# Kernel tuning notes

Hardware: AMD Instinct MI355X
Metric: run time of the kernel (lower is better)

The kernel has to match this reference:

```python
import jax, jax.numpy as jnp
import numpy as np

B = 12288
C = 1000


def setup_inputs() -> dict:
    key = jax.random.key(0)
    k1, k2 = jax.random.split(key)
    pred = jax.random.normal(k1, (B, C), dtype=jnp.float32)
    target = jax.random.randint(k2, (B,), 0, C)
    return {"pred": pred, "target": target, "num_classes": C}


def reference(pred, target, num_classes):
    # Vectorized form of the per-class loop: for a pair (b=negative, a=positive),
    # only class i = target[a] contributes, provided target[b] != target[a].
    #   margin[b, a] = pred[a, target[a]] - pred[b, target[a]]
    #   weight[b, a] = 1 / (N[target[b]] * N[target[a]])
    # loss = sum(hinge(margin) * weight) / (E * (E - 1)), E = #classes with N>0.
    N = jnp.zeros((num_classes,), jnp.float32).at[target].add(1.0)  # per-class counts
    E = jnp.sum(N > 0).astype(jnp.float32)  # exist_class_num
    f_own = jnp.take_along_axis(pred, target[:, None], axis=1)[:, 0]  # [B] pred[a, t[a]]
    P = pred[:, target]                      # [B, B]; P[b, a] = pred[b, target[a]]
    margin = f_own[None, :] - P              # [B_neg, B_pos]
    Nt = N[target]                            # [B] N[t[.]] (>= 1 always)
    diff = target[:, None] != target[None, :]  # t[b] != t[a]
    w = jnp.where(diff, 1.0 / (Nt[:, None] * Nt[None, :]), 0.0)
    loss = jnp.sum(jnp.maximum(1.0 - margin, 0.0) * w) / (E * (E - 1.0))
    return loss.reshape(1)
```

## Files before the change

kernel.cpp:

```cpp
#include <hip/hip_runtime.h>
#include <float.h>


#define CCLS 1000
#define PAD 64
#define LSLOT 32
#define TPB 1024
#define CCH 250
#define NCH 4
#define NRBLK 128
#define LSTR 257

__global__ __launch_bounds__(1024) void k_prep(const int* __restrict__ target, int B,
        int* ncnt, float* invN, int* fill, float* scal, int* flags) {
    __shared__ int h[CCLS];
    __shared__ int esh, mx;
    int tid = threadIdx.x;
    if (tid < CCLS) h[tid] = 0;
    if (tid == 0) { esh = 0; mx = 0; }
    __syncthreads();
    for (int j = tid; j < B; j += TPB) atomicAdd(&h[target[j]], 1);
    __syncthreads();
    if (tid < CCLS) {
        int n = h[tid];
        ncnt[tid] = n;
        invN[tid] = n ? 1.0f / (float)n : 0.f;
        fill[tid] = 0;
        if (n) atomicAdd(&esh, 1);
        atomicMax(&mx, n);
    }
    __syncthreads();
    if (tid == 0) {
        scal[0] = (float)esh;
        scal[1] = 0.f;
        flags[0] = 0;
        flags[1] = (mx > LSLOT - 1) ? 1 : 0;
    }
}

__global__ void k_scatter(const float* __restrict__ pred, const int* __restrict__ target,
                          int* fill, float* thrP, int B) {
    int j = blockIdx.x * 256 + threadIdx.x;
    if (j >= B) return;
    int tj = target[j];
    float fo = pred[(size_t)j * CCLS + tj];
    int pos = atomicAdd(&fill[tj], 1);
    if (pos < PAD) thrP[tj * PAD + pos] = fo - 1.0f;
}

__global__ __launch_bounds__(256) void k_sortpfx(const int* __restrict__ ncnt,
                                                 float* thrP, float* prefP) {
    int c = (blockIdx.x * 256 + threadIdx.x) >> 6;
    int lane = threadIdx.x & 63;
    if (c >= CCLS) return;
    int cnt = min(ncnt[c], PAD - 1);
    int base = c * PAD;
    float v = (lane < cnt) ? thrP[base + lane] : FLT_MAX;
    int rank = 0;
    float psum = 0.f, tot = 0.f;
    for (int k = 0; k < cnt; ++k) {
        float u = __shfl(v, k);
        bool sm = (u < v) || (u == v && k < lane);
        rank += sm ? 1 : 0;
        psum += sm ? u : 0.f;
        tot += u;
    }
    if (lane < cnt) { thrP[base + rank] = v; prefP[base + rank] = psum; }
    else           { thrP[base + lane] = FLT_MAX; prefP[base + lane] = tot; }
}

__global__ __launch_bounds__(TPB) void k_main(const float* __restrict__ pred,
        const int* __restrict__ target,
        const float* __restrict__ thrP, const float* __restrict__ prefP,
        const float* __restrict__ invN,
        float* scal, int* flags, float* __restrict__ out, int B, int RPB) {
    __shared__ float thrL[LSLOT][LSTR];
    __shared__ float prefL[LSLOT][LSTR];
    __shared__ float invNL[CCLS];
    __shared__ float redL[TPB / 64];

    const int tid = threadIdx.x;
    const int chunk = blockIdx.x / NRBLK;
    const int rblk = blockIdx.x % NRBLK;
    const int c0 = chunk * CCH;
    const int rbase = rblk * RPB;
    const int ovf = flags[1];

    for (int k = tid; k < CCLS; k += TPB) invNL[k] = invN[k];
    for (int g = tid; g < CCH * LSLOT; g += TPB) {
        int cc = g >> 5, k = g & 31;
        thrL[k][cc] = thrP[(size_t)(c0 + cc) * PAD + k];
        prefL[k][cc] = prefP[(size_t)(c0 + cc) * PAD + k];
    }
    __syncthreads();

    const int rr = tid >> 8;
    const int cc = tid & 255;
    const bool cvalid = cc < CCH;
    const int ccS = cvalid ? cc : 0;
    const int c = c0 + ccS;
    const float invc = cvalid ? invNL[c] : 0.f;

    const int rows = min(RPB, B - rbase);
    const int nit = (rows > rr) ? ((rows - rr + 3) >> 2) : 0;

    float acc = 0.f;
    if (!ovf) {
        const float e15 = thrL[15][ccS];
        const float e7  = thrL[7][ccS],  e23 = thrL[23][ccS];
        const float e3  = thrL[3][ccS],  e11 = thrL[11][ccS];
        const float e19 = thrL[19][ccS], e27 = thrL[27][ccS];
        const float e1  = thrL[1][ccS],  e5  = thrL[5][ccS];
        const float e9  = thrL[9][ccS],  e13 = thrL[13][ccS];
        const float e17 = thrL[17][ccS], e21 = thrL[21][ccS];
        const float e25 = thrL[25][ccS], e29 = thrL[29][ccS];
#pragma unroll 4
        for (int it = 0; it < nit; ++it) {
            const int i = rbase + it * 4 + rr;
            const int ti = target[i];
            const float p = pred[(size_t)i * CCLS + c];
            const bool b1 = e15 < p;
            const float t2 = b1 ? e23 : e7;
            const bool b2 = t2 < p;
            const float t3 = b1 ? (b2 ? e27 : e19) : (b2 ? e11 : e3);
            const bool b3 = t3 < p;
            const float t4 = b1 ? (b2 ? (b3 ? e29 : e25) : (b3 ? e21 : e17))
                                : (b2 ? (b3 ? e13 : e9)  : (b3 ? e5  : e1));
            const bool b4 = t4 < p;
            int lo = (b1 ? 16 : 0) + (b2 ? 8 : 0) + (b3 ? 4 : 0) + (b4 ? 2 : 0);
            lo += (thrL[lo][ccS] < p) ? 1 : 0;
            const float contrib = (float)lo * p - prefL[lo][ccS];
            const float w = (c != ti) ? invc * invNL[ti] : 0.f;
            acc = fmaf(contrib, w, acc);
        }
    } else {
        const float* seg = thrP + (size_t)c * PAD;
        const float* pseg = prefP + (size_t)c * PAD;
        for (int it = 0; it < nit; ++it) {
            const int i = rbase + it * 4 + rr;
            const int ti = target[i];
            const float p = pred[(size_t)i * CCLS + c];
            int lo = 0;
#pragma unroll
            for (int s = 32; s; s >>= 1) lo += (seg[lo + s - 1] < p) ? s : 0;
            const float contrib = (float)lo * p - pseg[lo];
            const float w = (c != ti) ? invc * invNL[ti] : 0.f;
            acc = fmaf(contrib, w, acc);
        }
    }

    for (int o = 32; o; o >>= 1) acc += __shfl_down(acc, o);
    if ((tid & 63) == 0) redL[tid >> 6] = acc;
    __syncthreads();
    if (tid == 0) {
        float ssum = 0.f;
#pragma unroll
        for (int k = 0; k < TPB / 64; ++k) ssum += redL[k];
        atomicAdd(&scal[1], ssum);
        __threadfence();
        int done = atomicAdd(&flags[0], 1);
        if (done == (int)gridDim.x - 1) {
            float tot = atomicAdd(&scal[1], 0.f);
            float E = scal[0];
            out[0] = tot / (E * (E - 1.0f));
        }
    }
}

extern "C" void kernel_launch(void* const* d_in, const int* in_sizes, int n_in,
                              void* d_out, int out_size, void* d_ws, size_t ws_size,
                              hipStream_t stream) {
    const float* pred = (const float*)d_in[0];
    const int* target = (const int*)d_in[1];
    const int B = in_sizes[1];

    char* ws = (char*)d_ws;
    int* ncnt    = (int*)(ws + 0);
    float* invN  = (float*)(ws + 4096);
    int* fill    = (int*)(ws + 8192);
    float* scal  = (float*)(ws + 12288);
    int* flags   = (int*)(ws + 12352);
    float* thrP  = (float*)(ws + 16384);
    float* prefP = (float*)(ws + 16384 + 262144);

    const int gb = (B + 255) / 256;
    const int RPB = (B + NRBLK - 1) / NRBLK;

    k_prep<<<1, TPB, 0, stream>>>(target, B, ncnt, invN, fill, scal, flags);
    k_scatter<<<gb, 256, 0, stream>>>(pred, target, fill, thrP, B);
    k_sortpfx<<<(CCLS * 64 + 255) / 256, 256, 0, stream>>>(ncnt, thrP, prefP);
    k_main<<<NCH * NRBLK, TPB, 0, stream>>>(pred, target, thrP, prefP, invN,
                                            scal, flags, (float*)d_out, B, RPB);
}
```

Measured before the change: 49.30 us.

## Interleave thresholds and prefix sums as float2, stage per-row weights in LDS

Thresholds and prefix sums are stored together as float2 pairs, so the final search step and the prefix lookup come from adjacent LDS slots. Per-row target and inverse count are staged once per block in shared memory instead of being reloaded from global memory each iteration. The main loop is manually batched four rows at a time, issuing all pred loads before the tree searches for more memory-level parallelism. Risks are higher register pressure and larger LDS use, and rows per block are capped at RMAX=256.

```diff
diff --git a/kernel.cpp b/kernel.cpp
--- a/kernel.cpp
+++ b/kernel.cpp
@@ -10,6 +10,7 @@
 #define NCH 4
 #define NRBLK 128
 #define LSTR 257
+#define RMAX 256
 
 __global__ __launch_bounds__(1024) void k_prep(const int* __restrict__ target, int B,
         int* ncnt, float* invN, int* fill, float* scal, int* flags) {
@@ -39,23 +40,23 @@
 }
 
 __global__ void k_scatter(const float* __restrict__ pred, const int* __restrict__ target,
-                          int* fill, float* thrP, int B) {
+                          int* fill, float2* pairP, int B) {
     int j = blockIdx.x * 256 + threadIdx.x;
     if (j >= B) return;
     int tj = target[j];
     float fo = pred[(size_t)j * CCLS + tj];
     int pos = atomicAdd(&fill[tj], 1);
-    if (pos < PAD) thrP[tj * PAD + pos] = fo - 1.0f;
+    if (pos < PAD) pairP[tj * PAD + pos] = make_float2(fo - 1.0f, 0.f);
 }
 
 __global__ __launch_bounds__(256) void k_sortpfx(const int* __restrict__ ncnt,
-                                                 float* thrP, float* prefP) {
+                                                 float2* pairP) {
     int c = (blockIdx.x * 256 + threadIdx.x) >> 6;
     int lane = threadIdx.x & 63;
     if (c >= CCLS) return;
     int cnt = min(ncnt[c], PAD - 1);
     int base = c * PAD;
-    float v = (lane < cnt) ? thrP[base + lane] : FLT_MAX;
+    float v = (lane < cnt) ? pairP[base + lane].x : FLT_MAX;
     int rank = 0;
     float psum = 0.f, tot = 0.f;
     for (int k = 0; k < cnt; ++k) {
@@ -65,18 +66,16 @@
         psum += sm ? u : 0.f;
         tot += u;
     }
-    if (lane < cnt) { thrP[base + rank] = v; prefP[base + rank] = psum; }
-    else           { thrP[base + lane] = FLT_MAX; prefP[base + lane] = tot; }
+    if (lane < cnt) pairP[base + rank] = make_float2(v, psum);
+    else            pairP[base + lane] = make_float2(FLT_MAX, tot);
 }
 
 __global__ __launch_bounds__(TPB) void k_main(const float* __restrict__ pred,
-        const int* __restrict__ target,
-        const float* __restrict__ thrP, const float* __restrict__ prefP,
+        const int* __restrict__ target, const float2* __restrict__ pairP,
         const float* __restrict__ invN,
         float* scal, int* flags, float* __restrict__ out, int B, int RPB) {
-    __shared__ float thrL[LSLOT][LSTR];
-    __shared__ float prefL[LSLOT][LSTR];
-    __shared__ float invNL[CCLS];
+    __shared__ float2 pairL[LSLOT][LSTR];
+    __shared__ float2 rowWT[RMAX];
     __shared__ float redL[TPB / 64];
 
     const int tid = threadIdx.x;
@@ -85,12 +84,15 @@
     const int c0 = chunk * CCH;
     const int rbase = rblk * RPB;
     const int ovf = flags[1];
-
-    for (int k = tid; k < CCLS; k += TPB) invNL[k] = invN[k];
+    const int rows = min(min(RPB, B - rbase), RMAX);
+
     for (int g = tid; g < CCH * LSLOT; g += TPB) {
         int cc = g >> 5, k = g & 31;
-        thrL[k][cc] = thrP[(size_t)(c0 + cc) * PAD + k];
-        prefL[k][cc] = prefP[(size_t)(c0 + cc) * PAD + k];
+        pairL[k][cc] = pairP[(size_t)(c0 + cc) * PAD + k];
+    }
+    for (int r = tid; r < rows; r += TPB) {
+        int t = target[rbase + r];
+        rowWT[r] = make_float2(__int_as_float(t), invN[t]);
     }
     __syncthreads();
 
@@ -99,26 +101,23 @@
     const bool cvalid = cc < CCH;
     const int ccS = cvalid ? cc : 0;
     const int c = c0 + ccS;
-    const float invc = cvalid ? invNL[c] : 0.f;
-
-    const int rows = min(RPB, B - rbase);
-    const int nit = (rows > rr) ? ((rows - rr + 3) >> 2) : 0;
+    const float invc = cvalid ? invN[c] : 0.f;
 
     float acc = 0.f;
     if (!ovf) {
-        const float e15 = thrL[15][ccS];
-        const float e7  = thrL[7][ccS],  e23 = thrL[23][ccS];
-        const float e3  = thrL[3][ccS],  e11 = thrL[11][ccS];
-        const float e19 = thrL[19][ccS], e27 = thrL[27][ccS];
-        const float e1  = thrL[1][ccS],  e5  = thrL[5][ccS];
-        const float e9  = thrL[9][ccS],  e13 = thrL[13][ccS];
-        const float e17 = thrL[17][ccS], e21 = thrL[21][ccS];
-        const float e25 = thrL[25][ccS], e29 = thrL[29][ccS];
-#pragma unroll 4
-        for (int it = 0; it < nit; ++it) {
-            const int i = rbase + it * 4 + rr;
-            const int ti = target[i];
-            const float p = pred[(size_t)i * CCLS + c];
+        float e1  = pairL[1][ccS].x,  e3  = pairL[3][ccS].x;
+        float e5  = pairL[5][ccS].x,  e7  = pairL[7][ccS].x;
+        float e9  = pairL[9][ccS].x,  e11 = pairL[11][ccS].x;
+        float e13 = pairL[13][ccS].x, e15 = pairL[15][ccS].x;
+        float e17 = pairL[17][ccS].x, e19 = pairL[19][ccS].x;
+        float e21 = pairL[21][ccS].x, e23 = pairL[23][ccS].x;
+        float e25 = pairL[25][ccS].x, e27 = pairL[27][ccS].x;
+        float e29 = pairL[29][ccS].x;
+        asm volatile("" : "+v"(e1), "+v"(e3), "+v"(e5), "+v"(e7), "+v"(e9),
+                          "+v"(e11), "+v"(e13), "+v"(e15), "+v"(e17), "+v"(e19),
+                          "+v"(e21), "+v"(e23), "+v"(e25), "+v"(e27), "+v"(e29));
+
+        auto tree = [&](float p) -> int {
             const bool b1 = e15 < p;
             const float t2 = b1 ? e23 : e7;
             const bool b2 = t2 < p;
@@ -127,24 +126,55 @@
             const float t4 = b1 ? (b2 ? (b3 ? e29 : e25) : (b3 ? e21 : e17))
                                 : (b2 ? (b3 ? e13 : e9)  : (b3 ? e5  : e1));
             const bool b4 = t4 < p;
-            int lo = (b1 ? 16 : 0) + (b2 ? 8 : 0) + (b3 ? 4 : 0) + (b4 ? 2 : 0);
-            lo += (thrL[lo][ccS] < p) ? 1 : 0;
-            const float contrib = (float)lo * p - prefL[lo][ccS];
-            const float w = (c != ti) ? invc * invNL[ti] : 0.f;
-            acc = fmaf(contrib, w, acc);
+            return (b1 ? 16 : 0) + (b2 ? 8 : 0) + (b3 ? 4 : 0) + (b4 ? 2 : 0);
+        };
+        auto fin = [&](float p, int lo, float2 qa, float2 qb, float2 wt) -> float {
+            const bool b5 = qa.x < p;
+            const float lof = (float)lo + (b5 ? 1.f : 0.f);
+            const float pf = b5 ? qb.y : qa.y;
+            const float contrib = lof * p - pf;
+            const int ti = __float_as_int(wt.x);
+            const float w = (c != ti) ? invc * wt.y : 0.f;
+            return contrib * w;
+        };
+
+        const float* pc = pred + c;
+        const int full = rows >> 4;
+        for (int it = 0; it < full; ++it) {
+            const int r0 = it * 16 + rr;
+            const float p0 = pc[(size_t)(rbase + r0)      * CCLS];
+            const float p1 = pc[(size_t)(rbase + r0 + 4)  * CCLS];
+            const float p2 = pc[(size_t)(rbase + r0 + 8)  * CCLS];
+            const float p3 = pc[(size_t)(rbase + r0 + 12) * CCLS];
+            const int l0 = tree(p0), l1 = tree(p1), l2 = tree(p2), l3 = tree(p3);
+            const float2 a0 = pairL[l0][ccS], q0 = pairL[l0 + 1][ccS];
+            const float2 a1 = pairL[l1][ccS], q1 = pairL[l1 + 1][ccS];
+            const float2 a2 = pairL[l2][ccS], q2 = pairL[l2 + 1][ccS];
+            const float2 a3 = pairL[l3][ccS], q3 = pairL[l3 + 1][ccS];
+            const float2 w0 = rowWT[r0],      w1 = rowWT[r0 + 4];
+            const float2 w2 = rowWT[r0 + 8],  w3 = rowWT[r0 + 12];
+            acc += fin(p0, l0, a0, q0, w0);
+            acc += fin(p1, l1, a1, q1, w1);
+            acc += fin(p2, l2, a2, q2, w2);
+            acc += fin(p3, l3, a3, q3, w3);
+        }
+        for (int r = full * 16 + rr; r < rows; r += 4) {
+            const float p = pc[(size_t)(rbase + r) * CCLS];
+            const int lo = tree(p);
+            const float2 qa = pairL[lo][ccS], qb = pairL[lo + 1][ccS];
+            acc += fin(p, lo, qa, qb, rowWT[r]);
         }
     } else {
-        const float* seg = thrP + (size_t)c * PAD;
-        const float* pseg = prefP + (size_t)c * PAD;
-        for (int it = 0; it < nit; ++it) {
-            const int i = rbase + it * 4 + rr;
-            const int ti = target[i];
-            const float p = pred[(size_t)i * CCLS + c];
+        const float2* seg = pairP + (size_t)c * PAD;
+        for (int r = rr; r < rows; r += 4) {
+            const float2 wt = rowWT[r];
+            const float p = pred[(size_t)(rbase + r) * CCLS + c];
             int lo = 0;
 #pragma unroll
-            for (int s = 32; s; s >>= 1) lo += (seg[lo + s - 1] < p) ? s : 0;
-            const float contrib = (float)lo * p - pseg[lo];
-            const float w = (c != ti) ? invc * invNL[ti] : 0.f;
+            for (int s = 32; s; s >>= 1) lo += (seg[lo + s - 1].x < p) ? s : 0;
+            const float contrib = (float)lo * p - seg[lo].y;
+            const int ti = __float_as_int(wt.x);
+            const float w = (c != ti) ? invc * wt.y : 0.f;
             acc = fmaf(contrib, w, acc);
         }
     }
@@ -180,15 +210,14 @@
     int* fill    = (int*)(ws + 8192);
     float* scal  = (float*)(ws + 12288);
     int* flags   = (int*)(ws + 12352);
-    float* thrP  = (float*)(ws + 16384);
-    float* prefP = (float*)(ws + 16384 + 262144);
+    float2* pairP = (float2*)(ws + 16384);
 
     const int gb = (B + 255) / 256;
     const int RPB = (B + NRBLK - 1) / NRBLK;
 
     k_prep<<<1, TPB, 0, stream>>>(target, B, ncnt, invN, fill, scal, flags);
-    k_scatter<<<gb, 256, 0, stream>>>(pred, target, fill, thrP, B);
-    k_sortpfx<<<(CCLS * 64 + 255) / 256, 256, 0, stream>>>(ncnt, thrP, prefP);
-    k_main<<<NCH * NRBLK, TPB, 0, stream>>>(pred, target, thrP, prefP, invN,
+    k_scatter<<<gb, 256, 0, stream>>>(pred, target, fill, pairP, B);
+    k_sortpfx<<<(CCLS * 64 + 255) / 256, 256, 0, stream>>>(ncnt, pairP);
+    k_main<<<NCH * NRBLK, TPB, 0, stream>>>(pred, target, pairP, invN,
                                             scal, flags, (float*)d_out, B, RPB);
 }
```

Result: slower. 132.1 us (+168.0%).

## Subtract same-class term algebraically and pack threshold/prefix pairs in LDS

Applied to the files above, without the earlier changes.

Drops the per-element same-class mask from the main loop. The same-class contribution is computed separately in the sort/prefix kernel, accumulated into a scalar and subtracted at the end. Thresholds and prefix sums are interleaved as float2, so the final two comparison steps use one float4 LDS read. Per-row weights are precomputed in shared memory, which removes the per-element target load and invN gather, and the class weight is factored out of the loop. This cuts per-element loads and ALU work, at the cost of one extra atomic per class and a possible float cancellation from the subtraction.

```diff
diff --git a/kernel.cpp b/kernel.cpp
--- a/kernel.cpp
+++ b/kernel.cpp
@@ -4,12 +4,12 @@
 
 #define CCLS 1000
 #define PAD 64
-#define LSLOT 32
 #define TPB 1024
 #define CCH 250
 #define NCH 4
 #define NRBLK 128
-#define LSTR 257
+#define CSTR 34
+#define RMAX 128
 
 __global__ __launch_bounds__(1024) void k_prep(const int* __restrict__ target, int B,
         int* ncnt, float* invN, int* fill, float* scal, int* flags) {
@@ -33,50 +33,59 @@
     if (tid == 0) {
         scal[0] = (float)esh;
         scal[1] = 0.f;
+        scal[2] = 0.f;
         flags[0] = 0;
-        flags[1] = (mx > LSLOT - 1) ? 1 : 0;
+        flags[1] = (mx > 31) ? 1 : 0;
     }
 }
 
 __global__ void k_scatter(const float* __restrict__ pred, const int* __restrict__ target,
-                          int* fill, float* thrP, int B) {
+                          int* fill, float2* pairP, int B) {
     int j = blockIdx.x * 256 + threadIdx.x;
     if (j >= B) return;
     int tj = target[j];
     float fo = pred[(size_t)j * CCLS + tj];
     int pos = atomicAdd(&fill[tj], 1);
-    if (pos < PAD) thrP[tj * PAD + pos] = fo - 1.0f;
+    if (pos < PAD) pairP[tj * PAD + pos] = make_float2(fo - 1.0f, 0.f);
 }
 
 __global__ __launch_bounds__(256) void k_sortpfx(const int* __restrict__ ncnt,
-                                                 float* thrP, float* prefP) {
+                                                 float2* pairP, float* scal) {
     int c = (blockIdx.x * 256 + threadIdx.x) >> 6;
     int lane = threadIdx.x & 63;
     if (c >= CCLS) return;
     int cnt = min(ncnt[c], PAD - 1);
     int base = c * PAD;
-    float v = (lane < cnt) ? thrP[base + lane] : FLT_MAX;
-    int rank = 0;
-    float psum = 0.f, tot = 0.f;
+    float v = (lane < cnt) ? pairP[base + lane].x : FLT_MAX;
+    float vp1 = v + 1.0f;
+    int rank = 0, rank2 = 0;
+    float psum = 0.f, tot = 0.f, psum2 = 0.f;
     for (int k = 0; k < cnt; ++k) {
         float u = __shfl(v, k);
         bool sm = (u < v) || (u == v && k < lane);
         rank += sm ? 1 : 0;
         psum += sm ? u : 0.f;
         tot += u;
-    }
-    if (lane < cnt) { thrP[base + rank] = v; prefP[base + rank] = psum; }
-    else           { thrP[base + lane] = FLT_MAX; prefP[base + lane] = tot; }
+        bool sm2 = (u < vp1);
+        rank2 += sm2 ? 1 : 0;
+        psum2 += sm2 ? u : 0.f;
+    }
+    if (lane < cnt) pairP[base + rank] = make_float2(v, psum);
+    else            pairP[base + lane] = make_float2(FLT_MAX, tot);
+    float F = (lane < cnt) ? ((float)rank2 * vp1 - psum2) : 0.f;
+    for (int o = 32; o; o >>= 1) F += __shfl_down(F, o);
+    if (lane == 0 && cnt > 0) {
+        float ic = 1.0f / (float)cnt;
+        atomicAdd(&scal[2], F * ic * ic);
+    }
 }
 
 __global__ __launch_bounds__(TPB) void k_main(const float* __restrict__ pred,
-        const int* __restrict__ target,
-        const float* __restrict__ thrP, const float* __restrict__ prefP,
+        const int* __restrict__ target, const float2* __restrict__ pairP,
         const float* __restrict__ invN,
         float* scal, int* flags, float* __restrict__ out, int B, int RPB) {
-    __shared__ float thrL[LSLOT][LSTR];
-    __shared__ float prefL[LSLOT][LSTR];
-    __shared__ float invNL[CCLS];
+    __shared__ float2 pairC[CCH][CSTR];
+    __shared__ float rowW[RMAX];
     __shared__ float redL[TPB / 64];
 
     const int tid = threadIdx.x;
@@ -85,13 +94,13 @@
     const int c0 = chunk * CCH;
     const int rbase = rblk * RPB;
     const int ovf = flags[1];
-
-    for (int k = tid; k < CCLS; k += TPB) invNL[k] = invN[k];
-    for (int g = tid; g < CCH * LSLOT; g += TPB) {
+    const int rows = min(min(RPB, B - rbase), RMAX);
+
+    for (int g = tid; g < CCH * 32; g += TPB) {
         int cc = g >> 5, k = g & 31;
-        thrL[k][cc] = thrP[(size_t)(c0 + cc) * PAD + k];
-        prefL[k][cc] = prefP[(size_t)(c0 + cc) * PAD + k];
-    }
+        pairC[cc][k] = pairP[(size_t)(c0 + cc) * PAD + k];
+    }
+    for (int r = tid; r < rows; r += TPB) rowW[r] = invN[target[rbase + r]];
     __syncthreads();
 
     const int rr = tid >> 8;
@@ -99,26 +108,26 @@
     const bool cvalid = cc < CCH;
     const int ccS = cvalid ? cc : 0;
     const int c = c0 + ccS;
-    const float invc = cvalid ? invNL[c] : 0.f;
-
-    const int rows = min(RPB, B - rbase);
+    const float invc = cvalid ? invN[c] : 0.f;
+
     const int nit = (rows > rr) ? ((rows - rr + 3) >> 2) : 0;
 
     float acc = 0.f;
     if (!ovf) {
-        const float e15 = thrL[15][ccS];
-        const float e7  = thrL[7][ccS],  e23 = thrL[23][ccS];
-        const float e3  = thrL[3][ccS],  e11 = thrL[11][ccS];
-        const float e19 = thrL[19][ccS], e27 = thrL[27][ccS];
-        const float e1  = thrL[1][ccS],  e5  = thrL[5][ccS];
-        const float e9  = thrL[9][ccS],  e13 = thrL[13][ccS];
-        const float e17 = thrL[17][ccS], e21 = thrL[21][ccS];
-        const float e25 = thrL[25][ccS], e29 = thrL[29][ccS];
-#pragma unroll 4
+        const volatile float* tf = (const volatile float*)&pairC[ccS][0];
+        const float e1  = tf[2],  e3  = tf[6],  e5  = tf[10], e7  = tf[14];
+        const float e9  = tf[18], e11 = tf[22], e13 = tf[26], e15 = tf[30];
+        const float e17 = tf[34], e19 = tf[38], e21 = tf[42], e23 = tf[46];
+        const float e25 = tf[50], e27 = tf[54], e29 = tf[58];
+
+        const char* ldsb = (const char*)&pairC[0][0] + ccS * (CSTR * 8);
+        const float* pp = pred + (size_t)(rbase + rr) * CCLS + c;
+
         for (int it = 0; it < nit; ++it) {
-            const int i = rbase + it * 4 + rr;
-            const int ti = target[i];
-            const float p = pred[(size_t)i * CCLS + c];
+            const float p = *pp;
+            pp += 4 * CCLS;
+            const float wt = rowW[it * 4 + rr];
+
             const bool b1 = e15 < p;
             const float t2 = b1 ? e23 : e7;
             const bool b2 = t2 < p;
@@ -127,27 +136,30 @@
             const float t4 = b1 ? (b2 ? (b3 ? e29 : e25) : (b3 ? e21 : e17))
                                 : (b2 ? (b3 ? e13 : e9)  : (b3 ? e5  : e1));
             const bool b4 = t4 < p;
-            int lo = (b1 ? 16 : 0) + (b2 ? 8 : 0) + (b3 ? 4 : 0) + (b4 ? 2 : 0);
-            lo += (thrL[lo][ccS] < p) ? 1 : 0;
-            const float contrib = (float)lo * p - prefL[lo][ccS];
-            const float w = (c != ti) ? invc * invNL[ti] : 0.f;
-            acc = fmaf(contrib, w, acc);
+            const int basep = (b1 ? 16 : 0) + (b2 ? 8 : 0) + (b3 ? 4 : 0) + (b4 ? 2 : 0);
+
+            const float4 q = *(const float4*)(ldsb + basep * 8);
+            const bool h0 = q.x < p;
+            const bool h1 = q.z < p;
+            const int k = basep + (h0 ? 1 : 0) + (h1 ? 1 : 0);
+            const float pf = h1 ? (q.w + q.z) : (h0 ? q.w : q.y);
+            const float contrib = fmaf((float)k, p, -pf);
+            acc = fmaf(contrib, wt, acc);
         }
     } else {
-        const float* seg = thrP + (size_t)c * PAD;
-        const float* pseg = prefP + (size_t)c * PAD;
+        const float2* seg = pairP + (size_t)c * PAD;
         for (int it = 0; it < nit; ++it) {
             const int i = rbase + it * 4 + rr;
-            const int ti = target[i];
             const float p = pred[(size_t)i * CCLS + c];
+            const float wt = rowW[it * 4 + rr];
             int lo = 0;
 #pragma unroll
-            for (int s = 32; s; s >>= 1) lo += (seg[lo + s - 1] < p) ? s : 0;
-            const float contrib = (float)lo * p - pseg[lo];
-            const float w = (c != ti) ? invc * invNL[ti] : 0.f;
-            acc = fmaf(contrib, w, acc);
+            for (int s = 32; s; s >>= 1) lo += (seg[lo + s - 1].x < p) ? s : 0;
+            const float contrib = (float)lo * p - seg[lo].y;
+            acc = fmaf(contrib, wt, acc);
         }
     }
+    acc *= invc;
 
     for (int o = 32; o; o >>= 1) acc += __shfl_down(acc, o);
     if ((tid & 63) == 0) redL[tid >> 6] = acc;
@@ -161,8 +173,9 @@
         int done = atomicAdd(&flags[0], 1);
         if (done == (int)gridDim.x - 1) {
             float tot = atomicAdd(&scal[1], 0.f);
+            float D = scal[2];
             float E = scal[0];
-            out[0] = tot / (E * (E - 1.0f));
+            out[0] = (tot - D) / (E * (E - 1.0f));
         }
     }
 }
@@ -180,15 +193,14 @@
     int* fill    = (int*)(ws + 8192);
     float* scal  = (float*)(ws + 12288);
     int* flags   = (int*)(ws + 12352);
-    float* thrP  = (float*)(ws + 16384);
-    float* prefP = (float*)(ws + 16384 + 262144);
+    float2* pairP = (float2*)(ws + 16384);
 
     const int gb = (B + 255) / 256;
     const int RPB = (B + NRBLK - 1) / NRBLK;
 
     k_prep<<<1, TPB, 0, stream>>>(target, B, ncnt, invN, fill, scal, flags);
-    k_scatter<<<gb, 256, 0, stream>>>(pred, target, fill, thrP, B);
-    k_sortpfx<<<(CCLS * 64 + 255) / 256, 256, 0, stream>>>(ncnt, thrP, prefP);
-    k_main<<<NCH * NRBLK, TPB, 0, stream>>>(pred, target, thrP, prefP, invN,
+    k_scatter<<<gb, 256, 0, stream>>>(pred, target, fill, pairP, B);
+    k_sortpfx<<<(CCLS * 64 + 255) / 256, 256, 0, stream>>>(ncnt, pairP, scal);
+    k_main<<<NCH * NRBLK, TPB, 0, stream>>>(pred, target, pairP, invN,
                                             scal, flags, (float*)d_out, B, RPB);
 }
```

Measured after the change: 64.29 us. +30.4%, slower.
